# Optimization experiments

Measured on AMD Instinct MI355X. Metric: run time of the kernel, lower is better.

## Reference

```python
import jax, jax.numpy as jnp
import numpy as np

B = 4096
D = 1024
WEIGHT = 1.0
EPS = 1e-7  # Keras K.epsilon()


def setup_inputs() -> dict:
    key = jax.random.key(0)
    k1, k2 = jax.random.split(key)
    return {
        "left": jax.random.normal(k1, (B, D), dtype=jnp.float32),
        "right": jax.random.normal(k2, (B, D), dtype=jnp.float32),
        "temperature": jnp.zeros((1,), dtype=jnp.float32),
    }


def _l2_normalize(x):
    # matches l2_norm: sqrt(max(sum(x^2), eps))
    sq = jnp.sum(jnp.square(x), axis=-1, keepdims=True)
    return x / jnp.sqrt(jnp.maximum(sq, EPS))


def reference(left, right, temperature):
    ln = _l2_normalize(left)   # [B, D]
    rn = _l2_normalize(right)  # [B, D]
    scale = jnp.exp(temperature)  # (1,) broadcasts
    logits_left = jnp.einsum("bd,cd->bc", ln, rn) * scale   # [B, B]
    logits_right = logits_left.T                             # rn @ ln.T * scale
    prob_left = jax.nn.softmax(logits_left, axis=-1)
    prob_right = jax.nn.softmax(logits_right, axis=-1)
    # NOTE: the original calls CCE(prob, labels), i.e. y_true=prob, y_pred=eye.
    # Keras clips y_pred to [eps, 1-eps]; loss = -sum(y_true * log(clip(y_pred))).
    labels = jnp.eye(B, dtype=jnp.float32)
    log_clipped = jnp.log(jnp.clip(labels, EPS, 1.0 - EPS))  # diag: log(1-eps), off: log(eps)
    loss_left = -jnp.sum(prob_left * log_clipped)
    loss_right = -jnp.sum(prob_right * log_clipped)
    loss = (loss_left + loss_right) / 2.0 / B
    return WEIGHT * loss
```

## Files before the change

kernel.cpp:

```cpp
#include <hip/hip_runtime.h>
#include <hip/hip_bf16.h>

#define Bn 4096
#define Dk 1024
#define EPSF 1e-7f

typedef float f32x4 __attribute__((ext_vector_type(4)));

__device__ __forceinline__ void async_copy16(const void* g, void* l) {
    __builtin_amdgcn_global_load_lds((__attribute__((address_space(1))) void*)(uintptr_t)g,
                                     (__attribute__((address_space(3))) void*)l, 16, 0, 0);
}

__global__ __launch_bounds__(256)
void nrm_kernel(const float4* __restrict__ left, const float4* __restrict__ right,
                unsigned* __restrict__ lnb8, unsigned* __restrict__ rnb8,
                float* __restrict__ diag, float* __restrict__ rowsum,
                float* __restrict__ colsum)
{
    const int row = blockIdx.x;
    const int t = threadIdx.x;
    const int idx = row * (Dk / 4) + t;
    const float4 l = left[idx];
    const float4 r = right[idx];
    float sl = l.x * l.x + l.y * l.y + l.z * l.z + l.w * l.w;
    float sr = r.x * r.x + r.y * r.y + r.z * r.z + r.w * r.w;
    float slr = l.x * r.x + l.y * r.y + l.z * r.z + l.w * r.w;
    #pragma unroll
    for (int off = 1; off < 64; off <<= 1) {
        sl += __shfl_xor(sl, off);
        sr += __shfl_xor(sr, off);
        slr += __shfl_xor(slr, off);
    }
    __shared__ float red[3][4];
    const int wave = t >> 6, lane = t & 63;
    if (lane == 0) { red[0][wave] = sl; red[1][wave] = sr; red[2][wave] = slr; }
    __syncthreads();
    sl = red[0][0] + red[0][1] + red[0][2] + red[0][3];
    sr = red[1][0] + red[1][1] + red[1][2] + red[1][3];
    const float invl = 1.0f / sqrtf(fmaxf(sl, EPSF));
    const float invr = 1.0f / sqrtf(fmaxf(sr, EPSF));
    const float sL = 8.0f * invl;
    const float sR = 8.0f * invr;
    int pkL = __builtin_amdgcn_cvt_pk_fp8_f32(l.x * sL, l.y * sL, 0, false);
    pkL = __builtin_amdgcn_cvt_pk_fp8_f32(l.z * sL, l.w * sL, pkL, true);
    int pkR = __builtin_amdgcn_cvt_pk_fp8_f32(r.x * sR, r.y * sR, 0, false);
    pkR = __builtin_amdgcn_cvt_pk_fp8_f32(r.z * sR, r.w * sR, pkR, true);
    lnb8[idx] = (unsigned)pkL;
    rnb8[idx] = (unsigned)pkR;
    if (t == 0) {
        const float d = red[2][0] + red[2][1] + red[2][2] + red[2][3];
        diag[row] = d * invl * invr;
        rowsum[row] = 0.f;
        colsum[row] = 0.f;
    }
}

__global__ __launch_bounds__(256, 2)
void gemm_sm_kernel(const unsigned char* __restrict__ lnb8,
                    const unsigned char* __restrict__ rnb8,
                    const float* __restrict__ temp,
                    float* __restrict__ rowsum, float* __restrict__ colsum)
{
    __shared__ __align__(16) unsigned char As[128 * 64];
    __shared__ __align__(16) unsigned char Bs[128 * 64];

    const int tid = threadIdx.x;
    const int wave = tid >> 6;
    const int lane = tid & 63;
    const int bm0 = blockIdx.y * 128;
    const int bn0 = blockIdx.x * 128;

    const int srow = lane >> 2;
    const int sj = lane & 3;
    int grow[2], gcol[2];
    unsigned char* lA[2];
    unsigned char* lB[2];
    #pragma unroll
    for (int i = 0; i < 2; ++i) {
        const int rloc = wave * 32 + i * 16 + srow;
        grow[i] = rloc;
        gcol[i] = 16 * (sj ^ ((rloc >> 1) & 3));
        lA[i] = As + (wave * 32 + i * 16) * 64;
        lB[i] = Bs + (wave * 32 + i * 16) * 64;
    }
    const unsigned char* baseA = lnb8 + (size_t)bm0 * Dk;
    const unsigned char* baseB = rnb8 + (size_t)bn0 * Dk;

    const int wm = (wave & 1) * 64;
    const int wn = (wave >> 1) * 64;
    const int quad = lane >> 4;
    const int r16 = lane & 15;
    const int key = r16 & 6;
    int aoff[4], boff[4];
    #pragma unroll
    for (int i = 0; i < 4; ++i) {
        aoff[i] = (wm + i * 16 + r16) * 64 + 8 * (quad ^ key);
        boff[i] = (wn + i * 16 + r16) * 64 + 8 * (quad ^ key);
    }
    const int ks1d = 8 * ((4 + quad) ^ key) - 8 * (quad ^ key);

    f32x4 acc[4][4];
    #pragma unroll
    for (int i = 0; i < 4; ++i)
        #pragma unroll
        for (int j = 0; j < 4; ++j)
            acc[i][j] = (f32x4){0.f, 0.f, 0.f, 0.f};

    for (int k0 = 0; k0 < Dk; k0 += 64) {
        #pragma unroll
        for (int i = 0; i < 2; ++i) {
            async_copy16(baseA + (size_t)grow[i] * Dk + k0 + gcol[i], lA[i]);
            async_copy16(baseB + (size_t)grow[i] * Dk + k0 + gcol[i], lB[i]);
        }
        __syncthreads();
        #pragma unroll
        for (int ks = 0; ks < 2; ++ks) {
            const int d = ks ? ks1d : 0;
            long af[4], bf[4];
            #pragma unroll
            for (int i = 0; i < 4; ++i) af[i] = *(const long*)(As + aoff[i] + d);
            #pragma unroll
            for (int i = 0; i < 4; ++i) bf[i] = *(const long*)(Bs + boff[i] + d);
            #pragma unroll
            for (int mi = 0; mi < 4; ++mi)
                #pragma unroll
                for (int ni = 0; ni < 4; ++ni)
                    acc[mi][ni] = __builtin_amdgcn_mfma_f32_16x16x32_fp8_fp8(
                        af[mi], bf[ni], acc[mi][ni], 0, 0, 0);
        }
        __syncthreads();
    }

    const float scale = __expf(temp[0]);
    const float dq = 0.015625f * scale;
    #pragma unroll
    for (int mi = 0; mi < 4; ++mi)
        #pragma unroll
        for (int ni = 0; ni < 4; ++ni)
            #pragma unroll
            for (int r = 0; r < 4; ++r)
                acc[mi][ni][r] = __expf(dq * acc[mi][ni][r] - scale);

    #pragma unroll
    for (int mi = 0; mi < 4; ++mi) {
        #pragma unroll
        for (int r = 0; r < 4; ++r) {
            float v = acc[mi][0][r] + acc[mi][1][r] + acc[mi][2][r] + acc[mi][3][r];
            v += __shfl_xor(v, 1);
            v += __shfl_xor(v, 2);
            v += __shfl_xor(v, 4);
            v += __shfl_xor(v, 8);
            if (r16 == 0)
                atomicAdd(&rowsum[bm0 + wm + mi * 16 + quad * 4 + r], v);
        }
    }
    #pragma unroll
    for (int ni = 0; ni < 4; ++ni) {
        float v = 0.f;
        #pragma unroll
        for (int mi = 0; mi < 4; ++mi)
            #pragma unroll
            for (int r = 0; r < 4; ++r)
                v += acc[mi][ni][r];
        v += __shfl_xor(v, 16);
        v += __shfl_xor(v, 32);
        if (quad == 0)
            atomicAdd(&colsum[bn0 + wn + ni * 16 + r16], v);
    }
}

__global__ __launch_bounds__(256)
void loss_kernel(const float* __restrict__ diag, const float* __restrict__ rowsum,
                 const float* __restrict__ colsum, const float* __restrict__ temp,
                 float* __restrict__ out)
{
    const int t = threadIdx.x;
    const float scale = __expf(temp[0]);
    float dL = 0.f, dR = 0.f;
    for (int i = t; i < Bn; i += 256) {
        const float e = __expf(scale * (diag[i] - 1.0f));
        dL += e * __builtin_amdgcn_rcpf(rowsum[i]);
        dR += e * __builtin_amdgcn_rcpf(colsum[i]);
    }
    #pragma unroll
    for (int off = 1; off < 64; off <<= 1) {
        dL += __shfl_xor(dL, off);
        dR += __shfl_xor(dR, off);
    }
    __shared__ float rd[2][4];
    const int wave = t >> 6, lane = t & 63;
    if (lane == 0) { rd[0][wave] = dL; rd[1][wave] = dR; }
    __syncthreads();
    if (t == 0) {
        dL = rd[0][0] + rd[0][1] + rd[0][2] + rd[0][3];
        dR = rd[1][0] + rd[1][1] + rd[1][2] + rd[1][3];
        const float logeps = logf(EPSF);
        const float log1m = logf(1.0f - EPSF);
        const float lossL = -(dL * log1m + ((float)Bn - dL) * logeps);
        const float lossR = -(dR * log1m + ((float)Bn - dR) * logeps);
        out[0] = (lossL + lossR) * 0.5f / (float)Bn;
    }
}

extern "C" void kernel_launch(void* const* d_in, const int* in_sizes, int n_in,
                              void* d_out, int out_size, void* d_ws, size_t ws_size,
                              hipStream_t stream) {
    (void)in_sizes; (void)n_in; (void)out_size; (void)ws_size;
    const float* left = (const float*)d_in[0];
    const float* right = (const float*)d_in[1];
    const float* temp = (const float*)d_in[2];

    char* ws = (char*)d_ws;
    unsigned char* lnb8 = (unsigned char*)ws;
    unsigned char* rnb8 = (unsigned char*)(ws + (size_t)Bn * Dk);
    float* diag = (float*)(ws + 2 * (size_t)Bn * Dk);
    float* rowsum = diag + Bn;
    float* colsum = rowsum + Bn;

    nrm_kernel<<<Bn, 256, 0, stream>>>((const float4*)left, (const float4*)right,
                                       (unsigned*)lnb8, (unsigned*)rnb8, diag, rowsum, colsum);
    dim3 g2(Bn / 128, Bn / 128);
    gemm_sm_kernel<<<g2, 256, 0, stream>>>(lnb8, rnb8, temp, rowsum, colsum);
    loss_kernel<<<1, 256, 0, stream>>>(diag, rowsum, colsum, temp, (float*)d_out);
}
```

Before: 128.1 us.

## Load GEMM fragments directly from global memory instead of staging through LDS

Result: slower. 205.1 us (+60.1%).

```diff
diff --git a/kernel.cpp b/kernel.cpp
--- a/kernel.cpp
+++ b/kernel.cpp
@@ -6,11 +6,6 @@
 #define EPSF 1e-7f
 
 typedef float f32x4 __attribute__((ext_vector_type(4)));
-
-__device__ __forceinline__ void async_copy16(const void* g, void* l) {
-    __builtin_amdgcn_global_load_lds((__attribute__((address_space(1))) void*)(uintptr_t)g,
-                                     (__attribute__((address_space(3))) void*)l, 16, 0, 0);
-}
 
 __global__ __launch_bounds__(256)
 void nrm_kernel(const float4* __restrict__ left, const float4* __restrict__ right,
@@ -62,43 +57,24 @@
                     const float* __restrict__ temp,
                     float* __restrict__ rowsum, float* __restrict__ colsum)
 {
-    __shared__ __align__(16) unsigned char As[128 * 64];
-    __shared__ __align__(16) unsigned char Bs[128 * 64];
-
     const int tid = threadIdx.x;
     const int wave = tid >> 6;
     const int lane = tid & 63;
     const int bm0 = blockIdx.y * 128;
     const int bn0 = blockIdx.x * 128;
 
-    const int srow = lane >> 2;
-    const int sj = lane & 3;
-    int grow[2], gcol[2];
-    unsigned char* lA[2];
-    unsigned char* lB[2];
-    #pragma unroll
-    for (int i = 0; i < 2; ++i) {
-        const int rloc = wave * 32 + i * 16 + srow;
-        grow[i] = rloc;
-        gcol[i] = 16 * (sj ^ ((rloc >> 1) & 3));
-        lA[i] = As + (wave * 32 + i * 16) * 64;
-        lB[i] = Bs + (wave * 32 + i * 16) * 64;
-    }
-    const unsigned char* baseA = lnb8 + (size_t)bm0 * Dk;
-    const unsigned char* baseB = rnb8 + (size_t)bn0 * Dk;
-
     const int wm = (wave & 1) * 64;
     const int wn = (wave >> 1) * 64;
     const int quad = lane >> 4;
     const int r16 = lane & 15;
-    const int key = r16 & 6;
-    int aoff[4], boff[4];
+
+    const unsigned char* pA[4];
+    const unsigned char* pB[4];
     #pragma unroll
     for (int i = 0; i < 4; ++i) {
-        aoff[i] = (wm + i * 16 + r16) * 64 + 8 * (quad ^ key);
-        boff[i] = (wn + i * 16 + r16) * 64 + 8 * (quad ^ key);
+        pA[i] = lnb8 + (size_t)(bm0 + wm + i * 16 + r16) * Dk + quad * 8;
+        pB[i] = rnb8 + (size_t)(bn0 + wn + i * 16 + r16) * Dk + quad * 8;
     }
-    const int ks1d = 8 * ((4 + quad) ^ key) - 8 * (quad ^ key);
 
     f32x4 acc[4][4];
     #pragma unroll
@@ -107,29 +83,24 @@
         for (int j = 0; j < 4; ++j)
             acc[i][j] = (f32x4){0.f, 0.f, 0.f, 0.f};
 
+    #pragma unroll 2
     for (int k0 = 0; k0 < Dk; k0 += 64) {
+        long af[2][4], bf[2][4];
         #pragma unroll
-        for (int i = 0; i < 2; ++i) {
-            async_copy16(baseA + (size_t)grow[i] * Dk + k0 + gcol[i], lA[i]);
-            async_copy16(baseB + (size_t)grow[i] * Dk + k0 + gcol[i], lB[i]);
-        }
-        __syncthreads();
+        for (int ks = 0; ks < 2; ++ks)
+            #pragma unroll
+            for (int i = 0; i < 4; ++i) {
+                af[ks][i] = *(const long*)(pA[i] + k0 + ks * 32);
+                bf[ks][i] = *(const long*)(pB[i] + k0 + ks * 32);
+            }
         #pragma unroll
-        for (int ks = 0; ks < 2; ++ks) {
-            const int d = ks ? ks1d : 0;
-            long af[4], bf[4];
-            #pragma unroll
-            for (int i = 0; i < 4; ++i) af[i] = *(const long*)(As + aoff[i] + d);
-            #pragma unroll
-            for (int i = 0; i < 4; ++i) bf[i] = *(const long*)(Bs + boff[i] + d);
+        for (int ks = 0; ks < 2; ++ks)
             #pragma unroll
             for (int mi = 0; mi < 4; ++mi)
                 #pragma unroll
                 for (int ni = 0; ni < 4; ++ni)
                     acc[mi][ni] = __builtin_amdgcn_mfma_f32_16x16x32_fp8_fp8(
-                        af[mi], bf[ni], acc[mi][ni], 0, 0, 0);
-        }
-        __syncthreads();
+                        af[ks][mi], bf[ks][ni], acc[mi][ni], 0, 0, 0);
     }
 
     const float scale = __expf(temp[0]);
```

## Double-buffer LDS tiles in FP8 GEMM to overlap loads with MFMA

Applied to the files above, without the earlier changes.

After: 119.1 us. 7.1% less time.

```diff
diff --git a/kernel.cpp b/kernel.cpp
--- a/kernel.cpp
+++ b/kernel.cpp
@@ -62,8 +62,8 @@
                     const float* __restrict__ temp,
                     float* __restrict__ rowsum, float* __restrict__ colsum)
 {
-    __shared__ __align__(16) unsigned char As[128 * 64];
-    __shared__ __align__(16) unsigned char Bs[128 * 64];
+    __shared__ __align__(16) unsigned char As[2][128 * 64];
+    __shared__ __align__(16) unsigned char Bs[2][128 * 64];
 
     const int tid = threadIdx.x;
     const int wave = tid >> 6;
@@ -73,16 +73,13 @@
 
     const int srow = lane >> 2;
     const int sj = lane & 3;
-    int grow[2], gcol[2];
-    unsigned char* lA[2];
-    unsigned char* lB[2];
+    int goff[2];
+    int lofs[2];
     #pragma unroll
     for (int i = 0; i < 2; ++i) {
         const int rloc = wave * 32 + i * 16 + srow;
-        grow[i] = rloc;
-        gcol[i] = 16 * (sj ^ ((rloc >> 1) & 3));
-        lA[i] = As + (wave * 32 + i * 16) * 64;
-        lB[i] = Bs + (wave * 32 + i * 16) * 64;
+        goff[i] = rloc * Dk + 16 * (sj ^ ((rloc >> 1) & 3));
+        lofs[i] = (wave * 32 + i * 16) * 64;
     }
     const unsigned char* baseA = lnb8 + (size_t)bm0 * Dk;
     const unsigned char* baseB = rnb8 + (size_t)bn0 * Dk;
@@ -107,21 +104,31 @@
         for (int j = 0; j < 4; ++j)
             acc[i][j] = (f32x4){0.f, 0.f, 0.f, 0.f};
 
-    for (int k0 = 0; k0 < Dk; k0 += 64) {
+    #pragma unroll
+    for (int i = 0; i < 2; ++i) {
+        async_copy16(baseA + goff[i], &As[0][lofs[i]]);
+        async_copy16(baseB + goff[i], &Bs[0][lofs[i]]);
+    }
+
+    #pragma unroll 2
+    for (int it = 0; it < 16; ++it) {
+        const int cur = it & 1;
+        const int nxt = cur ^ 1;
+        const int knext = ((it + 1) & 15) * 64;
         #pragma unroll
         for (int i = 0; i < 2; ++i) {
-            async_copy16(baseA + (size_t)grow[i] * Dk + k0 + gcol[i], lA[i]);
-            async_copy16(baseB + (size_t)grow[i] * Dk + k0 + gcol[i], lB[i]);
+            async_copy16(baseA + goff[i] + knext, &As[nxt][lofs[i]]);
+            async_copy16(baseB + goff[i] + knext, &Bs[nxt][lofs[i]]);
         }
-        __syncthreads();
+        asm volatile("s_waitcnt vmcnt(4)\n\ts_barrier" ::: "memory");
         #pragma unroll
         for (int ks = 0; ks < 2; ++ks) {
             const int d = ks ? ks1d : 0;
             long af[4], bf[4];
             #pragma unroll
-            for (int i = 0; i < 4; ++i) af[i] = *(const long*)(As + aoff[i] + d);
-            #pragma unroll
-            for (int i = 0; i < 4; ++i) bf[i] = *(const long*)(Bs + boff[i] + d);
+            for (int i = 0; i < 4; ++i) af[i] = *(const long*)(&As[cur][aoff[i] + d]);
+            #pragma unroll
+            for (int i = 0; i < 4; ++i) bf[i] = *(const long*)(&Bs[cur][boff[i] + d]);
             #pragma unroll
             for (int mi = 0; mi < 4; ++mi)
                 #pragma unroll
@@ -129,7 +136,7 @@
                     acc[mi][ni] = __builtin_amdgcn_mfma_f32_16x16x32_fp8_fp8(
                         af[mi], bf[ni], acc[mi][ni], 0, 0, 0);
         }
-        __syncthreads();
+        asm volatile("s_barrier" ::: "memory");
     }
 
     const float scale = __expf(temp[0]);
```
